# Performance work log

Hardware: AMD Instinct MI355X
Metric: run time of the kernel (lower is better)

The kernel has to match this reference:

```python
import jax, jax.numpy as jnp
import numpy as np

N, C, V, L = 32, 32, 400, 64
GH_IN, GH = 64, [128, 64]
NUM_GRAPHS, ORDER, K, ALPHA = 2, 2, 20, 0.05
OUT_CH = 32
CAT_CH = C * (NUM_GRAPHS * ORDER + 1)
BN_EPS = 1e-5


def setup_inputs() -> dict:
    key = jax.random.key(0)
    ks = jax.random.split(key, 12)
    s = lambda fan_in: 1.0 / np.sqrt(fan_in)
    return {
        "inputs": jax.random.normal(ks[0], (N, C, V, L), jnp.float32),
        "adj_mats": jax.random.normal(ks[1], (V, V, GH_IN), jnp.float32),
        # edge MLP: Linear(64->128), ReLU, Linear(128->64), ReLU, Linear(64->num_graphs)
        "mlp_w0": jax.random.normal(ks[2], (GH_IN, GH[0]), jnp.float32) * s(GH_IN),
        "mlp_b0": jnp.zeros((GH[0],), jnp.float32),
        "mlp_w1": jax.random.normal(ks[3], (GH[0], GH[1]), jnp.float32) * s(GH[0]),
        "mlp_b1": jnp.zeros((GH[1],), jnp.float32),
        "mlp_w2": jax.random.normal(ks[4], (GH[1], NUM_GRAPHS), jnp.float32) * s(GH[1]),
        "mlp_b2": jnp.zeros((NUM_GRAPHS,), jnp.float32),
        # 1x1 Conv2d(in=160, out=32) == channel-mixing matmul
        "conv_w": jax.random.normal(ks[5], (OUT_CH, CAT_CH), jnp.float32) * s(CAT_CH),
        "conv_b": jnp.zeros((OUT_CH,), jnp.float32),
        "bn_gamma": jnp.ones((OUT_CH,), jnp.float32),
        "bn_beta": jnp.zeros((OUT_CH,), jnp.float32),
    }


def _sparsify(logits):
    # logits: [V, V]; softmax over rows, keep top-K per row, renormalize.
    adj = jax.nn.softmax(logits, axis=1)
    _, idx = jax.lax.top_k(adj, K)                     # [V, K]
    mask = jnp.zeros((V, V), adj.dtype).at[jnp.arange(V)[:, None], idx].set(1.0)
    adj = adj * mask
    return adj / (adj.sum(axis=1, keepdims=True) + 1e-8)


def reference(inputs, adj_mats, mlp_w0, mlp_b0, mlp_w1, mlp_b1, mlp_w2, mlp_b2,
              conv_w, conv_b, bn_gamma, bn_beta):
    # edge MLP on [V, V, GH_IN] -> [V, V, NUM_GRAPHS]
    h = jax.nn.relu(adj_mats @ mlp_w0 + mlp_b0)
    h = jax.nn.relu(h @ mlp_w1 + mlp_b1)
    g = h @ mlp_w2 + mlp_b2
    A = jax.vmap(_sparsify)(jnp.moveaxis(g, 2, 0))     # [NUM_GRAPHS, V, V]

    x = jax.nn.relu(inputs)                            # [N, C, V, L]
    outs = [x]
    for i in range(NUM_GRAPHS):
        y = x
        for _ in range(ORDER):
            y = ALPHA * x + (1.0 - ALPHA) * jnp.einsum('ncvl,vw->ncwl', y, A[i])
            outs.append(y)
    x1 = jnp.concatenate(outs, axis=1)                 # [N, CAT_CH, V, L]
    out = jnp.einsum('ncvl,oc->novl', x1, conv_w) + conv_b[None, :, None, None]

    # BatchNorm2d, training mode (batch statistics, biased variance)
    mean = out.mean(axis=(0, 2, 3), keepdims=True)
    var = out.var(axis=(0, 2, 3), keepdims=True)
    out = (out - mean) * jax.lax.rsqrt(var + BN_EPS)
    out = out * bn_gamma[None, :, None, None] + bn_beta[None, :, None, None]
    return out
```

## Files before the change

kernel.cpp:

```cpp
#include <hip/hip_runtime.h>


#define VDIM 400
#define VP   416
#define KV   (4*VP)
#define EROWS (5*VP)
#define OL   2048
#define ALPHA_ 0.05f
#define BETA_  0.95f

typedef short  bf16x8 __attribute__((ext_vector_type(8)));
typedef float  f32x4  __attribute__((ext_vector_type(4)));

__device__ inline unsigned short f2bf(float x){
  unsigned int u = __float_as_uint(x);
  unsigned int r = (u + 0x7fffu + ((u >> 16) & 1u)) >> 16;
  return (unsigned short)r;
}
__device__ inline float bf2f(unsigned short u){
  return __uint_as_float(((unsigned int)u) << 16);
}

__global__ __launch_bounds__(256) void k_mlp3(
    const float* __restrict__ adj,
    const float* __restrict__ w0, const float* __restrict__ b0,
    const float* __restrict__ w1, const float* __restrict__ b1,
    const float* __restrict__ w2, const float* __restrict__ b2,
    float* __restrict__ g)
{
  __shared__ __align__(16) float s_in[64*68];
  __shared__ __align__(16) float s_h0[64*132];
  __shared__ __align__(16) float s_w [64*64];
  const int tid = threadIdx.x;
  const long ebase = (long)blockIdx.x * 64;
  const int eg = tid >> 4;
  const int ng = tid & 15;

  #pragma unroll
  for (int i = 0; i < 4; ++i){
    const int idx = tid + i*256;
    const int row = idx >> 4, f4 = (idx & 15)*4;
    *reinterpret_cast<f32x4*>(&s_in[row*68 + f4]) =
      *reinterpret_cast<const f32x4*>(&adj[(ebase + row)*64 + f4]);
  }
  #pragma unroll
  for (int i = 0; i < 4; ++i){
    const int idx = tid + i*256;
    const int f = idx >> 4, nn = (idx & 15)*4;
    *reinterpret_cast<f32x4*>(&s_w[f*64 + nn]) =
      *reinterpret_cast<const f32x4*>(&w0[f*128 + nn]);
  }
  __syncthreads();

  const f32x4 b0h0 = *reinterpret_cast<const f32x4*>(&b0[ng*4]);
  const f32x4 b0h1 = *reinterpret_cast<const f32x4*>(&b0[64 + ng*4]);
  const f32x4 b1v  = *reinterpret_cast<const f32x4*>(&b1[ng*4]);
  const f32x4 w2lo = *reinterpret_cast<const f32x4*>(&w2[ng*8]);
  const f32x4 w2hi = *reinterpret_cast<const f32x4*>(&w2[ng*8 + 4]);

  #pragma unroll
  for (int h = 0; h < 2; ++h){
    if (h == 1){
      __syncthreads();
      #pragma unroll
      for (int i = 0; i < 4; ++i){
        const int idx = tid + i*256;
        const int f = idx >> 4, nn = (idx & 15)*4;
        *reinterpret_cast<f32x4*>(&s_w[f*64 + nn]) =
          *reinterpret_cast<const f32x4*>(&w0[f*128 + 64 + nn]);
      }
      __syncthreads();
    }
    f32x4 acc[4];
    #pragma unroll
    for (int i = 0; i < 4; ++i) acc[i] = (f32x4){0.f,0.f,0.f,0.f};
    for (int f4 = 0; f4 < 64; f4 += 4){
      f32x4 wv0 = *reinterpret_cast<const f32x4*>(&s_w[(f4+0)*64 + ng*4]);
      f32x4 wv1 = *reinterpret_cast<const f32x4*>(&s_w[(f4+1)*64 + ng*4]);
      f32x4 wv2 = *reinterpret_cast<const f32x4*>(&s_w[(f4+2)*64 + ng*4]);
      f32x4 wv3 = *reinterpret_cast<const f32x4*>(&s_w[(f4+3)*64 + ng*4]);
      #pragma unroll
      for (int i = 0; i < 4; ++i){
        f32x4 av = *reinterpret_cast<const f32x4*>(&s_in[(eg*4+i)*68 + f4]);
        acc[i] += av.x*wv0 + av.y*wv1 + av.z*wv2 + av.w*wv3;
      }
    }
    const f32x4 bb = h ? b0h1 : b0h0;
    #pragma unroll
    for (int i = 0; i < 4; ++i){
      f32x4 v = acc[i] + bb;
      v.x = fmaxf(v.x, 0.f); v.y = fmaxf(v.y, 0.f);
      v.z = fmaxf(v.z, 0.f); v.w = fmaxf(v.w, 0.f);
      *reinterpret_cast<f32x4*>(&s_h0[(eg*4+i)*132 + h*64 + ng*4]) = v;
    }
  }
  __syncthreads();

  f32x4 acc1[4];
  #pragma unroll
  for (int i = 0; i < 4; ++i) acc1[i] = (f32x4){0.f,0.f,0.f,0.f};
  #pragma unroll
  for (int h = 0; h < 2; ++h){
    #pragma unroll
    for (int i = 0; i < 4; ++i){
      const int idx = tid + i*256;
      const int fr = idx >> 4, nn = (idx & 15)*4;
      *reinterpret_cast<f32x4*>(&s_w[fr*64 + nn]) =
        *reinterpret_cast<const f32x4*>(&w1[(h*64 + fr)*64 + nn]);
    }
    __syncthreads();
    for (int f4 = 0; f4 < 64; f4 += 4){
      f32x4 wv0 = *reinterpret_cast<const f32x4*>(&s_w[(f4+0)*64 + ng*4]);
      f32x4 wv1 = *reinterpret_cast<const f32x4*>(&s_w[(f4+1)*64 + ng*4]);
      f32x4 wv2 = *reinterpret_cast<const f32x4*>(&s_w[(f4+2)*64 + ng*4]);
      f32x4 wv3 = *reinterpret_cast<const f32x4*>(&s_w[(f4+3)*64 + ng*4]);
      #pragma unroll
      for (int i = 0; i < 4; ++i){
        f32x4 av = *reinterpret_cast<const f32x4*>(&s_h0[(eg*4+i)*132 + h*64 + f4]);
        acc1[i] += av.x*wv0 + av.y*wv1 + av.z*wv2 + av.w*wv3;
      }
    }
    __syncthreads();
  }

  float p0[4], p1[4];
  #pragma unroll
  for (int i = 0; i < 4; ++i){
    f32x4 hv = acc1[i] + b1v;
    hv.x = fmaxf(hv.x, 0.f); hv.y = fmaxf(hv.y, 0.f);
    hv.z = fmaxf(hv.z, 0.f); hv.w = fmaxf(hv.w, 0.f);
    p0[i] = hv.x*w2lo.x + hv.y*w2lo.z + hv.z*w2hi.x + hv.w*w2hi.z;
    p1[i] = hv.x*w2lo.y + hv.y*w2lo.w + hv.z*w2hi.y + hv.w*w2hi.w;
  }
  #pragma unroll
  for (int m = 8; m >= 1; m >>= 1){
    #pragma unroll
    for (int i = 0; i < 4; ++i){
      p0[i] += __shfl_xor(p0[i], m, 16);
      p1[i] += __shfl_xor(p1[i], m, 16);
    }
  }
  if (ng == 0){
    const float bb0 = b2[0], bb1 = b2[1];
    #pragma unroll
    for (int i = 0; i < 4; ++i){
      const long e = ebase + eg*4 + i;
      g[e*2 + 0] = p0[i] + bb0;
      g[e*2 + 1] = p1[i] + bb1;
    }
  }
}

__global__ __launch_bounds__(256) void k_sparsify(
    const float* __restrict__ g, float* __restrict__ Bf)
{
  const int row = blockIdx.x, gr = blockIdx.y, tid = threadIdx.x;
  const int wid = tid >> 6, lane = tid & 63;
  __shared__ float s_v[4]; __shared__ int s_i[4];
  __shared__ float s_p[512];
  __shared__ int   s_sel[512];
  const int i0 = tid, i1 = tid + 256;
  float v0 = (i0 < VDIM) ? g[(row*VDIM + i0)*2 + gr] : -3.4e38f;
  float v1 = (i1 < VDIM) ? g[(row*VDIM + i1)*2 + gr] : -3.4e38f;

  float m = fmaxf(v0, v1);
  for (int off = 32; off > 0; off >>= 1) m = fmaxf(m, __shfl_down(m, off, 64));
  if (lane == 0) s_v[wid] = m;
  __syncthreads();
  const float rowmax = fmaxf(fmaxf(s_v[0], s_v[1]), fmaxf(s_v[2], s_v[3]));
  float p0 = (i0 < VDIM) ? expf(v0 - rowmax) : 0.f;
  float p1 = (i1 < VDIM) ? expf(v1 - rowmax) : 0.f;
  float zs = p0 + p1;
  for (int off = 32; off > 0; off >>= 1) zs += __shfl_down(zs, off, 64);
  __syncthreads();
  if (lane == 0) s_v[wid] = zs;
  __syncthreads();
  const float Z = s_v[0] + s_v[1] + s_v[2] + s_v[3];
  p0 /= Z; p1 /= Z;
  s_p[i0] = p0; s_p[i1] = p1;
  s_sel[i0] = (i0 < VDIM) ? 0 : 1;
  s_sel[i1] = (i1 < VDIM) ? 0 : 1;
  __syncthreads();

  float ssum = 0.f;
  for (int it = 0; it < 20; ++it){
    float cv = -1.f; int ci = 0x7fffffff;
    if (!s_sel[i0])              { cv = p0; ci = i0; }
    if (!s_sel[i1] && (p1 > cv)) { cv = p1; ci = i1; }
    for (int off = 32; off > 0; off >>= 1){
      float ov = __shfl_down(cv, off, 64); int oi = __shfl_down(ci, off, 64);
      if (ov > cv || (ov == cv && oi < ci)){ cv = ov; ci = oi; }
    }
    if (lane == 0){ s_v[wid] = cv; s_i[wid] = ci; }
    __syncthreads();
    float wv = s_v[0]; int wi_ = s_i[0];
    #pragma unroll
    for (int k = 1; k < 4; ++k){
      float ov = s_v[k]; int oi = s_i[k];
      if (ov > wv || (ov == wv && oi < wi_)){ wv = ov; wi_ = oi; }
    }
    ssum += wv;
    if (tid == (wi_ & 255)) s_sel[wi_] = 1;
    __syncthreads();
  }
  const float inv = 1.0f / (ssum + 1e-8f);
  float* B1 = Bf + (size_t)(gr*2) * (VDIM*VDIM);
  if (i0 < VDIM) B1[(size_t)i0*VDIM + row] = s_sel[i0] ? (s_p[i0]*inv) : 0.f;
  if (i1 < VDIM) B1[(size_t)i1*VDIM + row] = s_sel[i1] ? (s_p[i1]*inv) : 0.f;
}

__global__ __launch_bounds__(256) void k_sq(float* __restrict__ Bf)
{
  const int gr = blockIdx.z;
  const float* S = Bf + (size_t)(2*gr)   * (VDIM*VDIM);
  float*       D = Bf + (size_t)(2*gr+1) * (VDIM*VDIM);
  const int tx = threadIdx.x & 15, ty = threadIdx.x >> 4;
  const int w = blockIdx.x*16 + ty, v = blockIdx.y*16 + tx;
  __shared__ float As[16][17], Bs[16][17];
  float acc = 0.f;
  for (int u0 = 0; u0 < VDIM; u0 += 16){
    As[ty][tx] = S[(size_t)w*VDIM + u0 + tx];
    Bs[ty][tx] = S[(size_t)(u0+ty)*VDIM + v];
    __syncthreads();
    #pragma unroll
    for (int u = 0; u < 16; ++u) acc += As[ty][u] * Bs[u][tx];
    __syncthreads();
  }
  D[(size_t)w*VDIM + v] = acc;
}

__global__ __launch_bounds__(256) void k_pack(
    const float* __restrict__ Bf, const float* __restrict__ conv_w,
    unsigned short* __restrict__ Bcat, unsigned short* __restrict__ Mpp,
    float* __restrict__ bns)
{
  const int idx = blockIdx.x*256 + threadIdx.x;
  if (idx < 512*KV){
    const int w = idx / KV, col = idx % KV;
    const int k1 = col / VP, v = col % VP;
    float val = (w < VDIM && v < VDIM) ? Bf[(size_t)k1*(VDIM*VDIM) + (size_t)w*VDIM + v] : 0.f;
    Bcat[idx] = f2bf(val);
  }
  if (blockIdx.x == 0){
    const float a = ALPHA_, b = BETA_;
    for (int mIdx = threadIdx.x; mIdx < 160*32; mIdx += 256){
      const int rowm = mIdx >> 5, c = mIdx & 31;
      const int k = rowm / 32, o = rowm & 31;
      float W[5];
      #pragma unroll
      for (int j = 0; j < 5; ++j) W[j] = conv_w[o*160 + j*32 + c];
      float val;
      if      (k == 0) val = W[0] + a*(W[1]+W[2]+W[3]+W[4]);
      else if (k == 1) val = b*W[1] + a*b*W[2];
      else if (k == 2) val = b*b*W[2];
      else if (k == 3) val = b*W[3] + a*b*W[4];
      else             val = b*b*W[4];
      Mpp[rowm*32 + c] = f2bf(val);
    }
    if (threadIdx.x < 64) bns[threadIdx.x] = 0.f;
  }
}

__global__ __launch_bounds__(640) void k_e(
    const float* __restrict__ x, const unsigned short* __restrict__ Mpp,
    unsigned short* __restrict__ e, int n0)
{
  const int v = blockIdx.x;
  const int n = n0 + blockIdx.y;
  const int tid = threadIdx.x;
  unsigned short* en = e + (size_t)blockIdx.y * EROWS * OL;
  if (v >= VDIM){
    for (int i = tid; i < 5*256; i += 640){
      const int k = i >> 8, off = (i & 255) * 8;
      *reinterpret_cast<uint4*>(&en[(size_t)(k*VP + v)*OL + off]) = make_uint4(0,0,0,0);
    }
    return;
  }
  __shared__ __align__(16) unsigned short s_xT[64*32];
  __shared__ __align__(16) unsigned short s_out[10*16*64];
  if (tid < 512){
    const int c = tid >> 4, l4 = (tid & 15) * 4;
    float4 xv = *reinterpret_cast<const float4*>(x + ((size_t)n*32 + c)*25600 + (size_t)v*64 + l4);
    s_xT[(l4+0)*32 + c] = f2bf(fmaxf(xv.x, 0.f));
    s_xT[(l4+1)*32 + c] = f2bf(fmaxf(xv.y, 0.f));
    s_xT[(l4+2)*32 + c] = f2bf(fmaxf(xv.z, 0.f));
    s_xT[(l4+3)*32 + c] = f2bf(fmaxf(xv.w, 0.f));
  }
  __syncthreads();
  const int wid = tid >> 6, lane = tid & 63;
  const int l15 = lane & 15, q = lane >> 4;
  const int m0 = wid * 16;
  bf16x8 afrag = *reinterpret_cast<const bf16x8*>(&Mpp[(m0 + l15)*32 + q*8]);
  const f32x4 zero = {0.f, 0.f, 0.f, 0.f};
  f32x4 acc[4];
  #pragma unroll
  for (int lt = 0; lt < 4; ++lt){
    bf16x8 bfrag = *reinterpret_cast<const bf16x8*>(&s_xT[(lt*16 + l15)*32 + q*8]);
    acc[lt] = __builtin_amdgcn_mfma_f32_16x16x32_bf16(afrag, bfrag, zero, 0, 0, 0);
  }
  unsigned short* so = &s_out[wid*1024];
  #pragma unroll
  for (int lt = 0; lt < 4; ++lt)
    #pragma unroll
    for (int r = 0; r < 4; ++r)
      so[(q*4 + r)*64 + lt*16 + l15] = f2bf(acc[lt][r]);
  const int k = wid >> 1, o0 = (wid & 1) * 16;
  const size_t gbase = (size_t)(k*VP + v)*OL + (size_t)o0*64;
  uint4 d0 = *reinterpret_cast<uint4*>(&so[lane*16]);
  uint4 d1 = *reinterpret_cast<uint4*>(&so[lane*16 + 8]);
  *reinterpret_cast<uint4*>(&en[gbase + lane*16])     = d0;
  *reinterpret_cast<uint4*>(&en[gbase + lane*16 + 8]) = d1;
}

__global__ __launch_bounds__(256) void k_prop(
    const unsigned short* __restrict__ Bcat, const unsigned short* __restrict__ e,
    const float* __restrict__ conv_b, float* __restrict__ out,
    float* __restrict__ bns, int n0)
{
  const int mt = blockIdx.x, nt = blockIdx.y, np = blockIdx.z;
  const int tid = threadIdx.x;
  const int wid = tid >> 6, lane = tid & 63;
  const int l15 = lane & 15, q = lane >> 4;
  const int ww = wid & 1, wh = wid >> 1;
  const unsigned short* en = e + (size_t)np * EROWS * OL;
  __shared__ __align__(16) unsigned short s_a[128*40];
  __shared__ __align__(16) unsigned short s_b[128*32];
  const f32x4 zero = {0.f, 0.f, 0.f, 0.f};
  f32x4 acc[4][4];
  #pragma unroll
  for (int mi = 0; mi < 4; ++mi)
    #pragma unroll
    for (int ni = 0; ni < 4; ++ni) acc[mi][ni] = zero;
  const int w_base = mt*128, ol0 = nt*128;

  for (int kk = 0; kk < KV; kk += 32){
    #pragma unroll
    for (int i = 0; i < 2; ++i){
      const int idx = tid + i*256;
      const int m = idx >> 2, seg = idx & 3;
      uint4 d = *reinterpret_cast<const uint4*>(&Bcat[(size_t)(w_base + m)*KV + kk + seg*8]);
      *reinterpret_cast<uint4*>(&s_a[m*40 + seg*8]) = d;
    }
    #pragma unroll
    for (int i = 0; i < 2; ++i){
      const int idx = tid + i*256;
      const int r = idx >> 4, seg = idx & 15;
      union { uint4 u; unsigned short s[8]; } d;
      d.u = *reinterpret_cast<const uint4*>(&en[(size_t)(VP + kk + r)*OL + ol0 + seg*8]);
      const int kb = r >> 3, kin = r & 7;
      #pragma unroll
      for (int t = 0; t < 8; ++t){
        const int nn = seg*8 + t;
        s_b[nn*32 + ((kb ^ ((nn >> 3) & 3)) << 3) + kin] = d.s[t];
      }
    }
    __syncthreads();
    bf16x8 af[4], bfr[4];
    #pragma unroll
    for (int mi = 0; mi < 4; ++mi){
      const int m = ww*64 + mi*16 + l15;
      af[mi] = *reinterpret_cast<const bf16x8*>(&s_a[m*40 + q*8]);
    }
    #pragma unroll
    for (int ni = 0; ni < 4; ++ni){
      const int nn = wh*64 + ni*16 + l15;
      bfr[ni] = *reinterpret_cast<const bf16x8*>(&s_b[nn*32 + ((q ^ ((nn >> 3) & 3)) << 3)]);
    }
    #pragma unroll
    for (int mi = 0; mi < 4; ++mi)
      #pragma unroll
      for (int ni = 0; ni < 4; ++ni)
        acc[mi][ni] = __builtin_amdgcn_mfma_f32_16x16x32_bf16(af[mi], bfr[ni], acc[mi][ni], 0, 0, 0);
    __syncthreads();
  }

  const int n_g = n0 + np;
  const int o = (ol0 >> 6) + wh;
  const float cb = conv_b[o];
  float bsum = 0.f, bsq = 0.f;
  #pragma unroll
  for (int mi = 0; mi < 4; ++mi){
    #pragma unroll
    for (int ni = 0; ni < 4; ++ni){
      const int nloc = wh*64 + ni*16 + l15;
      const int ol = ol0 + nloc;
      const int l = ol & 63;
      #pragma unroll
      for (int r = 0; r < 4; ++r){
        const int w = w_base + ww*64 + mi*16 + q*4 + r;
        if (w < VDIM){
          float val = acc[mi][ni][r] + bf2f(en[(size_t)w*OL + ol]) + cb;
          out[(((size_t)n_g*32 + o)*VDIM + w)*64 + l] = val;
          bsum += val; bsq += val*val;
        }
      }
    }
  }
  for (int off = 32; off > 0; off >>= 1){
    bsum += __shfl_down(bsum, off, 64);
    bsq  += __shfl_down(bsq,  off, 64);
  }
  if (lane == 0){
    atomicAdd(&bns[o], bsum);
    atomicAdd(&bns[32 + o], bsq);
  }
}

__global__ __launch_bounds__(256) void k_bnapply(
    float* __restrict__ out, const float* __restrict__ bns,
    const float* __restrict__ gamma, const float* __restrict__ beta, int total4)
{
  const int idx = blockIdx.x*256 + threadIdx.x;
  if (idx >= total4) return;
  const int o = (int)(((long)idx*4 / 25600) & 31);
  const float invM = 1.f / 819200.f;
  const float mean = bns[o] * invM;
  const float var  = bns[32+o] * invM - mean*mean;
  const float inv  = 1.0f / sqrtf(var + 1e-5f);
  const float sc = inv * gamma[o];
  const float sh = beta[o] - mean * sc;
  float4 v = reinterpret_cast<float4*>(out)[idx];
  v.x = v.x*sc + sh; v.y = v.y*sc + sh; v.z = v.z*sc + sh; v.w = v.w*sc + sh;
  reinterpret_cast<float4*>(out)[idx] = v;
}

extern "C" void kernel_launch(void* const* d_in, const int* in_sizes, int n_in,
                              void* d_out, int out_size, void* d_ws, size_t ws_size,
                              hipStream_t stream)
{
  const float* x      = (const float*)d_in[0];
  const float* adj    = (const float*)d_in[1];
  const float* w0     = (const float*)d_in[2];
  const float* b0     = (const float*)d_in[3];
  const float* w1     = (const float*)d_in[4];
  const float* b1     = (const float*)d_in[5];
  const float* w2     = (const float*)d_in[6];
  const float* b2     = (const float*)d_in[7];
  const float* conv_w = (const float*)d_in[8];
  const float* conv_b = (const float*)d_in[9];
  const float* gamma  = (const float*)d_in[10];
  const float* beta   = (const float*)d_in[11];
  float* out = (float*)d_out;

  char* ws = (char*)d_ws;
  size_t off = 0;
  auto alloc = [&](size_t bytes) -> void* {
    void* p = ws + off;
    off = (off + bytes + 255) & ~(size_t)255;
    return p;
  };
  float*          g_   = (float*)         alloc((size_t)VDIM*VDIM*2*4);
  float*          Bf   = (float*)         alloc((size_t)4*VDIM*VDIM*4);
  unsigned short* Bcat = (unsigned short*)alloc((size_t)512*KV*2);
  unsigned short* Mpp  = (unsigned short*)alloc((size_t)160*32*2);
  float*          bns  = (float*)         alloc((size_t)64*4);
  const size_t per_n = (size_t)EROWS * OL * 2;
  size_t avail = (ws_size > off) ? (ws_size - off) : 0;
  int NC = (int)(avail / per_n);
  if (NC > 8) NC = 8;
  if (NC < 1) NC = 1;
  while (32 % NC) NC--;
  unsigned short* ebuf = (unsigned short*)(ws + off);

  k_mlp3<<<2500, 256, 0, stream>>>(adj, w0, b0, w1, b1, w2, b2, g_);
  k_sparsify<<<dim3(VDIM, 2), 256, 0, stream>>>(g_, Bf);
  k_sq<<<dim3(25, 25, 2), 256, 0, stream>>>(Bf);
  k_pack<<<(512*KV + 255)/256, 256, 0, stream>>>(Bf, conv_w, Bcat, Mpp, bns);
  for (int n0 = 0; n0 < 32; n0 += NC){
    k_e<<<dim3(VP, NC), 640, 0, stream>>>(x, Mpp, ebuf, n0);
    k_prop<<<dim3(4, 16, NC), 256, 0, stream>>>(Bcat, ebuf, conv_b, out, bns, n0);
  }
  k_bnapply<<<(26214400/4 + 255)/256, 256, 0, stream>>>(out, bns, gamma, beta, 26214400/4);
}
```

Baseline: 786.9 us.

## Restructure edge MLP kernel to split hidden units across waves with wave-uniform weights

```diff
diff --git a/kernel.cpp b/kernel.cpp
--- a/kernel.cpp
+++ b/kernel.cpp
@@ -28,126 +28,99 @@
     const float* __restrict__ w2, const float* __restrict__ b2,
     float* __restrict__ g)
 {
-  __shared__ __align__(16) float s_in[64*68];
-  __shared__ __align__(16) float s_h0[64*132];
-  __shared__ __align__(16) float s_w [64*64];
-  const int tid = threadIdx.x;
+  __shared__ __align__(16) float s_inT[64*68];
+  __shared__ __align__(16) float s_h1 [64*72];
+  __shared__ __align__(16) float s_red[4*64*2];
+  const int tid  = threadIdx.x;
   const long ebase = (long)blockIdx.x * 64;
-  const int eg = tid >> 4;
-  const int ng = tid & 15;
+  const int wid  = __builtin_amdgcn_readfirstlane(tid >> 6);
+  const int lane = tid & 63;
 
   #pragma unroll
   for (int i = 0; i < 4; ++i){
     const int idx = tid + i*256;
     const int row = idx >> 4, f4 = (idx & 15)*4;
-    *reinterpret_cast<f32x4*>(&s_in[row*68 + f4]) =
-      *reinterpret_cast<const f32x4*>(&adj[(ebase + row)*64 + f4]);
-  }
-  #pragma unroll
-  for (int i = 0; i < 4; ++i){
-    const int idx = tid + i*256;
-    const int f = idx >> 4, nn = (idx & 15)*4;
-    *reinterpret_cast<f32x4*>(&s_w[f*64 + nn]) =
-      *reinterpret_cast<const f32x4*>(&w0[f*128 + nn]);
-  }
-  __syncthreads();
-
-  const f32x4 b0h0 = *reinterpret_cast<const f32x4*>(&b0[ng*4]);
-  const f32x4 b0h1 = *reinterpret_cast<const f32x4*>(&b0[64 + ng*4]);
-  const f32x4 b1v  = *reinterpret_cast<const f32x4*>(&b1[ng*4]);
-  const f32x4 w2lo = *reinterpret_cast<const f32x4*>(&w2[ng*8]);
-  const f32x4 w2hi = *reinterpret_cast<const f32x4*>(&w2[ng*8 + 4]);
-
-  #pragma unroll
-  for (int h = 0; h < 2; ++h){
-    if (h == 1){
-      __syncthreads();
+    f32x4 v = *reinterpret_cast<const f32x4*>(&adj[(ebase + row)*64 + f4]);
+    s_inT[(f4+0)*68 + row] = v.x;
+    s_inT[(f4+1)*68 + row] = v.y;
+    s_inT[(f4+2)*68 + row] = v.z;
+    s_inT[(f4+3)*68 + row] = v.w;
+  }
+  __syncthreads();
+
+  const int n0 = wid * 32;
+  float h0[32];
+  #pragma unroll
+  for (int j = 0; j < 32; ++j) h0[j] = b0[n0 + j];
+  #pragma unroll 2
+  for (int f = 0; f < 64; ++f){
+    const float a = s_inT[f*68 + lane];
+    const float* __restrict__ wr = &w0[f*128 + n0];
+    #pragma unroll
+    for (int j = 0; j < 32; ++j) h0[j] = fmaf(a, wr[j], h0[j]);
+  }
+  #pragma unroll
+  for (int j = 0; j < 32; ++j) h0[j] = fmaxf(h0[j], 0.f);
+
+  float p[64];
+  #pragma unroll
+  for (int nh = 0; nh < 2; ++nh){
+    float acc1[32];
+    #pragma unroll
+    for (int j = 0; j < 32; ++j) acc1[j] = 0.f;
+    #pragma unroll 2
+    for (int f = 0; f < 32; ++f){
+      const float hv = h0[f];
+      const float* __restrict__ wr = &w1[(n0 + f)*64 + nh*32];
       #pragma unroll
-      for (int i = 0; i < 4; ++i){
-        const int idx = tid + i*256;
-        const int f = idx >> 4, nn = (idx & 15)*4;
-        *reinterpret_cast<f32x4*>(&s_w[f*64 + nn]) =
-          *reinterpret_cast<const f32x4*>(&w0[f*128 + 64 + nn]);
+      for (int j = 0; j < 32; ++j) acc1[j] = fmaf(hv, wr[j], acc1[j]);
+    }
+    #pragma unroll
+    for (int j = 0; j < 32; ++j) p[nh*32 + j] = acc1[j];
+  }
+
+  #pragma unroll
+  for (int w = 0; w < 4; ++w){
+    if (wid == w){
+      if (w == 0){
+        #pragma unroll
+        for (int j = 0; j < 64; j += 4){
+          f32x4 v = { p[j] + b1[j],   p[j+1] + b1[j+1],
+                      p[j+2] + b1[j+2], p[j+3] + b1[j+3] };
+          *reinterpret_cast<f32x4*>(&s_h1[lane*72 + j]) = v;
+        }
+      } else {
+        #pragma unroll
+        for (int j = 0; j < 64; j += 4){
+          f32x4 v = *reinterpret_cast<f32x4*>(&s_h1[lane*72 + j]);
+          v.x += p[j]; v.y += p[j+1]; v.z += p[j+2]; v.w += p[j+3];
+          *reinterpret_cast<f32x4*>(&s_h1[lane*72 + j]) = v;
+        }
       }
-      __syncthreads();
-    }
-    f32x4 acc[4];
-    #pragma unroll
-    for (int i = 0; i < 4; ++i) acc[i] = (f32x4){0.f,0.f,0.f,0.f};
-    for (int f4 = 0; f4 < 64; f4 += 4){
-      f32x4 wv0 = *reinterpret_cast<const f32x4*>(&s_w[(f4+0)*64 + ng*4]);
-      f32x4 wv1 = *reinterpret_cast<const f32x4*>(&s_w[(f4+1)*64 + ng*4]);
-      f32x4 wv2 = *reinterpret_cast<const f32x4*>(&s_w[(f4+2)*64 + ng*4]);
-      f32x4 wv3 = *reinterpret_cast<const f32x4*>(&s_w[(f4+3)*64 + ng*4]);
-      #pragma unroll
-      for (int i = 0; i < 4; ++i){
-        f32x4 av = *reinterpret_cast<const f32x4*>(&s_in[(eg*4+i)*68 + f4]);
-        acc[i] += av.x*wv0 + av.y*wv1 + av.z*wv2 + av.w*wv3;
-      }
-    }
-    const f32x4 bb = h ? b0h1 : b0h0;
-    #pragma unroll
-    for (int i = 0; i < 4; ++i){
-      f32x4 v = acc[i] + bb;
-      v.x = fmaxf(v.x, 0.f); v.y = fmaxf(v.y, 0.f);
-      v.z = fmaxf(v.z, 0.f); v.w = fmaxf(v.w, 0.f);
-      *reinterpret_cast<f32x4*>(&s_h0[(eg*4+i)*132 + h*64 + ng*4]) = v;
-    }
-  }
-  __syncthreads();
-
-  f32x4 acc1[4];
-  #pragma unroll
-  for (int i = 0; i < 4; ++i) acc1[i] = (f32x4){0.f,0.f,0.f,0.f};
-  #pragma unroll
-  for (int h = 0; h < 2; ++h){
-    #pragma unroll
-    for (int i = 0; i < 4; ++i){
-      const int idx = tid + i*256;
-      const int fr = idx >> 4, nn = (idx & 15)*4;
-      *reinterpret_cast<f32x4*>(&s_w[fr*64 + nn]) =
-        *reinterpret_cast<const f32x4*>(&w1[(h*64 + fr)*64 + nn]);
-    }
-    __syncthreads();
-    for (int f4 = 0; f4 < 64; f4 += 4){
-      f32x4 wv0 = *reinterpret_cast<const f32x4*>(&s_w[(f4+0)*64 + ng*4]);
-      f32x4 wv1 = *reinterpret_cast<const f32x4*>(&s_w[(f4+1)*64 + ng*4]);
-      f32x4 wv2 = *reinterpret_cast<const f32x4*>(&s_w[(f4+2)*64 + ng*4]);
-      f32x4 wv3 = *reinterpret_cast<const f32x4*>(&s_w[(f4+3)*64 + ng*4]);
-      #pragma unroll
-      for (int i = 0; i < 4; ++i){
-        f32x4 av = *reinterpret_cast<const f32x4*>(&s_h0[(eg*4+i)*132 + h*64 + f4]);
-        acc1[i] += av.x*wv0 + av.y*wv1 + av.z*wv2 + av.w*wv3;
-      }
-    }
-    __syncthreads();
-  }
-
-  float p0[4], p1[4];
-  #pragma unroll
-  for (int i = 0; i < 4; ++i){
-    f32x4 hv = acc1[i] + b1v;
-    hv.x = fmaxf(hv.x, 0.f); hv.y = fmaxf(hv.y, 0.f);
-    hv.z = fmaxf(hv.z, 0.f); hv.w = fmaxf(hv.w, 0.f);
-    p0[i] = hv.x*w2lo.x + hv.y*w2lo.z + hv.z*w2hi.x + hv.w*w2hi.z;
-    p1[i] = hv.x*w2lo.y + hv.y*w2lo.w + hv.z*w2hi.y + hv.w*w2hi.w;
-  }
-  #pragma unroll
-  for (int m = 8; m >= 1; m >>= 1){
-    #pragma unroll
-    for (int i = 0; i < 4; ++i){
-      p0[i] += __shfl_xor(p0[i], m, 16);
-      p1[i] += __shfl_xor(p1[i], m, 16);
-    }
-  }
-  if (ng == 0){
-    const float bb0 = b2[0], bb1 = b2[1];
-    #pragma unroll
-    for (int i = 0; i < 4; ++i){
-      const long e = ebase + eg*4 + i;
-      g[e*2 + 0] = p0[i] + bb0;
-      g[e*2 + 1] = p1[i] + bb1;
-    }
+    }
+    __syncthreads();
+  }
+
+  float q0 = 0.f, q1 = 0.f;
+  #pragma unroll
+  for (int j = 0; j < 16; ++j){
+    const int n = wid*16 + j;
+    const float hv = fmaxf(s_h1[lane*72 + n], 0.f);
+    q0 = fmaf(hv, w2[n*2 + 0], q0);
+    q1 = fmaf(hv, w2[n*2 + 1], q1);
+  }
+  s_red[(wid*64 + lane)*2 + 0] = q0;
+  s_red[(wid*64 + lane)*2 + 1] = q1;
+  __syncthreads();
+  if (wid == 0){
+    float r0 = b2[0], r1 = b2[1];
+    #pragma unroll
+    for (int w = 0; w < 4; ++w){
+      r0 += s_red[(w*64 + lane)*2 + 0];
+      r1 += s_red[(w*64 + lane)*2 + 1];
+    }
+    g[(ebase + lane)*2 + 0] = r0;
+    g[(ebase + lane)*2 + 1] = r1;
   }
 }
 
```

Measured after the change: 778.3 us. Within noise of the previous version (-1.1%).
